# Kernel optimization log

Hardware: AMD Instinct MI355X
Metric: run time of the kernel (lower is better)

Reference implementation:

```python
import jax, jax.numpy as jnp
import numpy as np

N, E, D, H, C, ED = 30000, 300000, 256, 8, 32, 32
HID = H * C  # 256 = hidden_channels


def setup_inputs() -> dict:
    key = jax.random.key(0)
    ks = jax.random.split(key, 14)
    w = lambda k, shp, fan: (jax.random.normal(k, shp, jnp.float32) / np.sqrt(fan)).astype(jnp.float32)
    return {
        "x": jax.random.normal(ks[0], (N, D), jnp.float32),
        "edge_index": jax.random.randint(ks[1], (2, E), 0, N, jnp.int32),
        "edge_attr": jax.random.normal(ks[2], (E, ED), jnp.float32),
        # TransformerConv params (PyG: q/k/v Linears have bias; lin_edge & lin_skip bias=False)
        "Wq": w(ks[3], (D, HID), D), "bq": 0.01 * jax.random.normal(ks[4], (HID,), jnp.float32),
        "Wk": w(ks[5], (D, HID), D), "bk": 0.01 * jax.random.normal(ks[6], (HID,), jnp.float32),
        "Wv": w(ks[7], (D, HID), D), "bv": 0.01 * jax.random.normal(ks[8], (HID,), jnp.float32),
        "We": w(ks[9], (ED, HID), ED),
        "Wskip": w(ks[10], (D, HID), D),
        # MLP([HID, HID, HID], gelu-tanh, plain_last=False): two Linear+act layers
        "W1": w(ks[11], (HID, HID), HID), "b1": jnp.zeros((HID,), jnp.float32),
        "W2": w(ks[12], (HID, HID), HID), "b2": jnp.zeros((HID,), jnp.float32),
    }


def reference(x, edge_index, edge_attr, Wq, bq, Wk, bk, Wv, bv, We, Wskip, W1, b1, W2, b2):
    src, dst = edge_index[0], edge_index[1]  # message flows src -> dst
    q = (x @ Wq + bq).reshape(N, H, C)
    k = (x @ Wk + bk).reshape(N, H, C)
    v = (x @ Wv + bv).reshape(N, H, C)
    e = (edge_attr @ We).reshape(E, H, C)
    k_e = k[src] + e                               # [E,H,C]
    v_e = v[src] + e                               # [E,H,C]
    logits = jnp.einsum('ehc,ehc->eh', q[dst], k_e) / np.sqrt(C)  # [E,H]
    # segment softmax over incoming edges of each dst node
    m = jax.ops.segment_max(logits, dst, num_segments=N)          # [N,H]
    a = jnp.exp(logits - m[dst])
    denom = jax.ops.segment_sum(a, dst, num_segments=N)           # [N,H]
    alpha = a / (denom[dst] + 1e-16)                              # [E,H]
    agg = jax.ops.segment_sum(alpha[:, :, None] * v_e, dst, num_segments=N)  # [N,H,C]
    out = agg.reshape(N, HID) + x @ Wskip          # concat heads + root skip
    # residual MLP: x + gelu(gelu(x W1 + b1) W2 + b2)
    h = jax.nn.gelu(out @ W1 + b1, approximate=True)
    h = jax.nn.gelu(h @ W2 + b2, approximate=True)
    return out + h
```

## Files before the change

kernel.cpp:

```cpp
#include <hip/hip_runtime.h>

#define NN 30000
#define NE 300000
#define HIDDEN 256

typedef __attribute__((ext_vector_type(8))) __bf16 bf16x8;
typedef __attribute__((ext_vector_type(4))) __bf16 bf16x4;
typedef __attribute__((ext_vector_type(4))) float float4v;

__device__ inline __bf16 f2bf(float f) {
  unsigned u = __builtin_bit_cast(unsigned, f);
  u += 0x7fffu + ((u >> 16) & 1u);
  unsigned short s = (unsigned short)(u >> 16);
  return __builtin_bit_cast(__bf16, s);
}
__device__ inline float bf2f(__bf16 b) {
  unsigned short s = __builtin_bit_cast(unsigned short, b);
  unsigned u = ((unsigned)s) << 16;
  return __builtin_bit_cast(float, u);
}
__device__ inline float gelu_tanh(float x) {
  float x3 = x * x * x;
  return 0.5f * x * (1.0f + tanhf(0.79788456080286536f * (x + 0.044715f * x3)));
}

#define PREP_XB_END (1829 + (NN * 32 + 255) / 256)
__global__ __launch_bounds__(256) void prep_kernel(
    const float* __restrict__ Wq, const float* __restrict__ Wk, const float* __restrict__ Wv,
    const float* __restrict__ Wsk, const float* __restrict__ W1, const float* __restrict__ W2,
    const float* __restrict__ We, const float* __restrict__ bq, const float* __restrict__ bk,
    const float* __restrict__ bv, const float* __restrict__ x,
    __bf16* __restrict__ WTall, __bf16* __restrict__ WT1, __bf16* __restrict__ WT2,
    float* __restrict__ ball, float* __restrict__ WeT, __bf16* __restrict__ xb,
    int* __restrict__ degz) {
  const int b = blockIdx.x;
  const int tid = threadIdx.x;
  if (b < 1792) {
    const int region = b >> 8;
    const int idx = ((b & 255) << 8) | tid;
    const int k = idx & 255, n = idx >> 8;
    float v;
    if (region == 3) {
      const int h = n >> 5, d = n & 31;
      const float* wq = Wq + (size_t)k * 256 + h * 32;
      const float* we = We + (size_t)d * 256 + h * 32;
      float s = 0.f;
#pragma unroll
      for (int c = 0; c < 32; ++c) s += wq[c] * we[c];
      v = s;
    } else {
      const float* W = (region == 0) ? Wq : (region == 1) ? Wk : (region == 2) ? Wv
                     : (region == 4) ? Wsk : (region == 5) ? W1 : W2;
      v = W[(size_t)k * 256 + n];
    }
    const __bf16 bv16 = f2bf(v);
    if (region < 5) WTall[(size_t)region * 65536 + idx] = bv16;
    else if (region == 5) WT1[idx] = bv16;
    else WT2[idx] = bv16;
  } else if (b < 1797) {
    const int j = (b - 1792) * 256 + tid;
    if (j < 1280) {
      float v = 0.f;
      if (j < 256) v = bq[j];
      else if (j < 512) v = bk[j - 256];
      else if (j < 768) v = bv[j - 512];
      else if (j < 1024) {
        const int col = j - 768, h = col >> 5, d = col & 31;
        const float* bqh = bq + h * 32;
        const float* we = We + (size_t)d * 256 + h * 32;
        float s = 0.f;
#pragma unroll
        for (int c = 0; c < 32; ++c) s += bqh[c] * we[c];
        v = s;
      }
      ball[j] = v;
    }
  } else if (b < 1829) {
    const int idx = (b - 1797) * 256 + tid;
    const int ch = idx >> 5, d = idx & 31;
    WeT[idx] = We[(size_t)d * 256 + ch];
  } else if (b < PREP_XB_END) {
    const int t = (b - 1829) * 256 + tid;
    if (t < NN * 256 / 8) {
      const float* p = x + (size_t)t * 8;
      float4v f0 = *(const float4v*)(p);
      float4v f1 = *(const float4v*)(p + 4);
      bf16x8 o;
#pragma unroll
      for (int j = 0; j < 4; ++j) { o[j] = f2bf(f0[j]); o[j + 4] = f2bf(f1[j]); }
      *(bf16x8*)(xb + (size_t)t * 8) = o;
    }
  } else {
    const int idx = (b - PREP_XB_END) * 256 + tid;
    if (idx < 2 * NN) degz[idx] = 0;
  }
}

__global__ void count_deg_kernel(const int* __restrict__ dst, int* __restrict__ deg, int E) {
  int e = blockIdx.x * 256 + threadIdx.x;
  if (e < E) atomicAdd(&deg[dst[e]], 1);
}

__global__ __launch_bounds__(256) void offs_fused_kernel(const int* __restrict__ deg,
                                                         int* __restrict__ offs, int n) {
  __shared__ int tmp[256];
  __shared__ int sbase[4];
  const int t = threadIdx.x;
  const int lim = blockIdx.x * 256;
  int bp = 0;
  for (int idx = t; idx < lim; idx += 256) bp += deg[idx];
#pragma unroll
  for (int s = 1; s < 64; s <<= 1) bp += __shfl_xor(bp, s);
  if ((t & 63) == 0) sbase[t >> 6] = bp;
  const int i = lim + t;
  int v = (i < n) ? deg[i] : 0;
  tmp[t] = v;
  __syncthreads();
  const int base = sbase[0] + sbase[1] + sbase[2] + sbase[3];
  for (int s = 1; s < 256; s <<= 1) {
    int u = (t >= s) ? tmp[t - s] : 0;
    __syncthreads();
    tmp[t] += u;
    __syncthreads();
  }
  if (i < n) offs[i] = base + tmp[t] - v;
  if (blockIdx.x == gridDim.x - 1 && t == 0) offs[n] = NE;
}

__global__ void scatter_kernel(const int* __restrict__ srcIn, const int* __restrict__ dstIn,
                               const float* __restrict__ ea,
                               const int* __restrict__ offs, int* __restrict__ cursor,
                               int* __restrict__ srcs, __bf16* __restrict__ eaC, int E) {
  int e = blockIdx.x * 256 + threadIdx.x;
  if (e >= E) return;
  const float* src = ea + (size_t)e * 32;
  float4v f[8];
#pragma unroll
  for (int t = 0; t < 8; ++t) f[t] = *(const float4v*)(src + t * 4);
  int d = dstIn[e];
  int p = atomicAdd(&cursor[d], 1);
  int o = offs[d] + p;
  srcs[o] = srcIn[e];
  __bf16* dstp = eaC + (size_t)o * 32;
#pragma unroll
  for (int t = 0; t < 4; ++t) {
    bf16x8 b;
#pragma unroll
    for (int j = 0; j < 4; ++j) { b[j] = f2bf(f[t * 2][j]); b[j + 4] = f2bf(f[t * 2 + 1][j]); }
    *(bf16x8*)(dstp + t * 8) = b;
  }
}

template <int GX, int EPI, int MODE>
__global__ __launch_bounds__(256) void gemm_k4(
    const __bf16* __restrict__ A, const __bf16* __restrict__ Wt,
    const float* __restrict__ bias,
    float* __restrict__ Yf, __bf16* __restrict__ Ybf,
    __bf16* __restrict__ QGp, __bf16* __restrict__ KVp,
    const float* __restrict__ resid, int M, int gyTiles) {
  __shared__ char smem[128 * 264 * 2];
  __bf16* Bs = (__bf16*)smem;
  const int bid = blockIdx.x;
  const int stripe = bid / (8 * GX);
  const int rem = bid % (8 * GX);
  const int y8 = rem % 8;
  const int xt = rem / 8;
  const int y = stripe * 8 + y8;
  if (y >= gyTiles) return;
  const int n0 = xt * 128;

  {
    const int t = threadIdx.x;
#pragma unroll
    for (int i = 0; i < 16; ++i) {
      int g = i * 256 + t;
      int row = g >> 5;
      int c16 = g & 31;
      bf16x8 v = *(const bf16x8*)(Wt + (size_t)(n0 + row) * 256 + c16 * 8);
      *(bf16x8*)(Bs + row * 264 + c16 * 8) = v;
    }
  }
  __syncthreads();

  const int lane = threadIdx.x & 63;
  const int w = threadIdx.x >> 6;
  const int r = lane & 15;
  const int q = lane >> 4;
  const int mw = y * 128 + w * 32;
  int ar0 = mw + r;      if (ar0 >= M) ar0 = M - 1;
  int ar1 = mw + 16 + r; if (ar1 >= M) ar1 = M - 1;
  const int kq = q * 8;

  float4v acc[2][8];
#pragma unroll
  for (int i = 0; i < 2; ++i)
#pragma unroll
    for (int t = 0; t < 8; ++t) acc[i][t] = (float4v){0.f, 0.f, 0.f, 0.f};

#pragma unroll
  for (int kk = 0; kk < 256; kk += 32) {
    const int ka = kk + kq;
    bf16x8 a0 = *(const bf16x8*)(A + (size_t)ar0 * 256 + ka);
    bf16x8 a1 = *(const bf16x8*)(A + (size_t)ar1 * 256 + ka);
    bf16x8 b[8];
#pragma unroll
    for (int t = 0; t < 8; ++t)
      b[t] = *(const bf16x8*)(Bs + (t * 16 + r) * 264 + ka);
#pragma unroll
    for (int t = 0; t < 8; ++t) {
      acc[0][t] = __builtin_amdgcn_mfma_f32_16x16x32_bf16(a0, b[t], acc[0][t], 0, 0, 0);
      acc[1][t] = __builtin_amdgcn_mfma_f32_16x16x32_bf16(a1, b[t], acc[1][t], 0, 0, 0);
    }
  }
  __syncthreads();

  float* cs = (float*)smem + w * 4224;
#pragma unroll
  for (int t = 0; t < 8; ++t) {
    const int col = n0 + t * 16 + r;
    const float bb = bias ? bias[col] : 0.0f;
#pragma unroll
    for (int i2 = 0; i2 < 2; ++i2)
#pragma unroll
      for (int ii = 0; ii < 4; ++ii) {
        float v = acc[i2][t][ii] + bb;
        if constexpr (EPI == 2 || EPI == 3) v = gelu_tanh(v);
        cs[(i2 * 16 + q * 4 + ii) * 132 + t * 16 + r] = v;
      }
  }

  constexpr int NSTR = GX * 128;
  const int p = n0 >> 8;
  const int cbase = n0 & 255;
  __bf16* dstI = (p == 0 || p == 3) ? QGp : KVp;
  const int moff = (p >= 2) ? 4 : 0;
#pragma unroll
  for (int i = 0; i < 16; ++i) {
    const int rl = i * 2 + (lane >> 5);
    const int row = mw + rl;
    const int c4 = (lane & 31) * 4;
    float4v v = *(const float4v*)(cs + rl * 132 + c4);
    if (row < M) {
      if constexpr (MODE == 1) {
        if (p == 4) {
          *(float4v*)(Yf + (size_t)row * 256 + cbase + c4) = v;
        } else {
          bf16x4 b4;
          b4[0] = f2bf(v[0]); b4[1] = f2bf(v[1]); b4[2] = f2bf(v[2]); b4[3] = f2bf(v[3]);
          const int c = cbase + c4;
          *(bf16x4*)(dstI + (size_t)row * 512 + 2 * c + moff) = b4;
        }
      } else if constexpr (EPI == 1) {
        *(float4v*)(Yf + (size_t)row * NSTR + n0 + c4) = v;
      } else if constexpr (EPI == 3) {
        float4v rr = *(const float4v*)(resid + (size_t)row * NSTR + n0 + c4);
        v[0] += rr[0]; v[1] += rr[1]; v[2] += rr[2]; v[3] += rr[3];
        *(float4v*)(Yf + (size_t)row * NSTR + n0 + c4) = v;
      } else {
        bf16x4 b4;
        b4[0] = f2bf(v[0]); b4[1] = f2bf(v[1]); b4[2] = f2bf(v[2]); b4[3] = f2bf(v[3]);
        *(bf16x4*)(Ybf + (size_t)row * NSTR + n0 + c4) = b4;
      }
    }
  }
}

__global__ __launch_bounds__(256) void attn_kernel(
    const __bf16* __restrict__ QG, const __bf16* __restrict__ KV,
    const __bf16* __restrict__ eaC,
    const int* __restrict__ srcs, const int* __restrict__ offs,
    float* __restrict__ OUT, __bf16* __restrict__ AE) {
  __shared__ float sdn[4][64];
  __shared__ float sav[4][64][4], sae[4][64][4];
  const int lane = threadIdx.x & 63;
  const int w = threadIdx.x >> 6;
  const int n = blockIdx.x;
  const int sub = lane & 7;
  const int ch = w * 64 + lane;

  const int beg = offs[n], end = offs[n + 1];
  const float opre = OUT[(size_t)n * 256 + ch];

  const float LSC = 0.25506589858f;
  const bf16x8 qg = *(const bf16x8*)(QG + (size_t)n * 512 + lane * 8);
  const float q0 = bf2f(qg[0]) * LSC, q1 = bf2f(qg[1]) * LSC;
  const float q2 = bf2f(qg[2]) * LSC, q3 = bf2f(qg[3]) * LSC;
  const float g0 = bf2f(qg[4]) * LSC, g1 = bf2f(qg[5]) * LSC;
  const float g2 = bf2f(qg[6]) * LSC, g3 = bf2f(qg[7]) * LSC;

  float denom = 0.f;
  float4v accv = {0.f, 0.f, 0.f, 0.f};
  float4v acce = {0.f, 0.f, 0.f, 0.f};

  for (int b0 = beg; b0 < end; b0 += 64) {
    const int rem = end - b0;
    const int cnt = (rem < 64) ? rem : 64;
    const int sl = (lane < cnt) ? lane : cnt - 1;
    const int myS = srcs[b0 + sl];

    int j = w;
    for (; j + 4 < cnt; j += 8) {
      const int s0 = __builtin_amdgcn_readlane(myS, j);
      const int s1 = __builtin_amdgcn_readlane(myS, j + 4);
      const bf16x8 kv0 = *(const bf16x8*)(KV + (size_t)s0 * 512 + lane * 8);
      const bf16x4 a0 = *(const bf16x4*)(eaC + (size_t)(b0 + j) * 32 + sub * 4);
      const bf16x8 kv1 = *(const bf16x8*)(KV + (size_t)s1 * 512 + lane * 8);
      const bf16x4 a1 = *(const bf16x4*)(eaC + (size_t)(b0 + j + 4) * 32 + sub * 4);
      const float e00 = bf2f(a0[0]), e01 = bf2f(a0[1]), e02 = bf2f(a0[2]), e03 = bf2f(a0[3]);
      const float e10 = bf2f(a1[0]), e11 = bf2f(a1[1]), e12 = bf2f(a1[2]), e13 = bf2f(a1[3]);
      float p0 = q0 * bf2f(kv0[0]) + q1 * bf2f(kv0[1]) + q2 * bf2f(kv0[2]) + q3 * bf2f(kv0[3])
               + g0 * e00 + g1 * e01 + g2 * e02 + g3 * e03;
      float p1 = q0 * bf2f(kv1[0]) + q1 * bf2f(kv1[1]) + q2 * bf2f(kv1[2]) + q3 * bf2f(kv1[3])
               + g0 * e10 + g1 * e11 + g2 * e12 + g3 * e13;
      p0 += __shfl_xor(p0, 1); p1 += __shfl_xor(p1, 1);
      p0 += __shfl_xor(p0, 2); p1 += __shfl_xor(p1, 2);
      p0 += __shfl_xor(p0, 4); p1 += __shfl_xor(p1, 4);
      const float w0 = exp2f(p0);
      const float w1 = exp2f(p1);
      denom += w0 + w1;
      accv[0] += w0 * bf2f(kv0[4]) + w1 * bf2f(kv1[4]);
      accv[1] += w0 * bf2f(kv0[5]) + w1 * bf2f(kv1[5]);
      accv[2] += w0 * bf2f(kv0[6]) + w1 * bf2f(kv1[6]);
      accv[3] += w0 * bf2f(kv0[7]) + w1 * bf2f(kv1[7]);
      acce[0] += w0 * e00 + w1 * e10;
      acce[1] += w0 * e01 + w1 * e11;
      acce[2] += w0 * e02 + w1 * e12;
      acce[3] += w0 * e03 + w1 * e13;
    }
    if (j < cnt) {
      const int s0 = __builtin_amdgcn_readlane(myS, j);
      const bf16x8 kv0 = *(const bf16x8*)(KV + (size_t)s0 * 512 + lane * 8);
      const bf16x4 a0 = *(const bf16x4*)(eaC + (size_t)(b0 + j) * 32 + sub * 4);
      const float e00 = bf2f(a0[0]), e01 = bf2f(a0[1]), e02 = bf2f(a0[2]), e03 = bf2f(a0[3]);
      float p0 = q0 * bf2f(kv0[0]) + q1 * bf2f(kv0[1]) + q2 * bf2f(kv0[2]) + q3 * bf2f(kv0[3])
               + g0 * e00 + g1 * e01 + g2 * e02 + g3 * e03;
      p0 += __shfl_xor(p0, 1);
      p0 += __shfl_xor(p0, 2);
      p0 += __shfl_xor(p0, 4);
      const float w0 = exp2f(p0);
      denom += w0;
      accv[0] += w0 * bf2f(kv0[4]);
      accv[1] += w0 * bf2f(kv0[5]);
      accv[2] += w0 * bf2f(kv0[6]);
      accv[3] += w0 * bf2f(kv0[7]);
      acce[0] += w0 * e00;
      acce[1] += w0 * e01;
      acce[2] += w0 * e02;
      acce[3] += w0 * e03;
    }
  }

  sdn[w][lane] = denom;
#pragma unroll
  for (int j = 0; j < 4; ++j) { sav[w][lane][j] = accv[j]; sae[w][lane][j] = acce[j]; }
  __syncthreads();

  const int lp = ch >> 2, jp = ch & 3;
  const float D = sdn[0][lp] + sdn[1][lp] + sdn[2][lp] + sdn[3][lp];
  const float av = sav[0][lp][jp] + sav[1][lp][jp] + sav[2][lp][jp] + sav[3][lp][jp];
  const float ae = sae[0][lp][jp] + sae[1][lp][jp] + sae[2][lp][jp] + sae[3][lp][jp];
  const float inv = 1.0f / (D + 1e-16f);
  OUT[(size_t)n * 256 + ch] = opre + av * inv;
  AE[(size_t)n * 256 + ch] = f2bf(ae * inv);
}

__global__ __launch_bounds__(256) void post_kernel(
    const __bf16* __restrict__ AE, const float* __restrict__ WeT,
    float* __restrict__ OUT, __bf16* __restrict__ OUTh) {
  const int lane = threadIdx.x & 63;
  const int wave = threadIdx.x >> 6;
  const int c0 = lane * 4;
  const int hg = lane >> 3;

  float4v w4[4][8];
#pragma unroll
  for (int j = 0; j < 4; ++j)
#pragma unroll
    for (int s = 0; s < 8; ++s)
      w4[j][s] = *(const float4v*)(WeT + (size_t)(c0 + j) * 32 + s * 4);

  const int nbase = blockIdx.x * 64;
  for (int it = 0; it < 16; ++it) {
    const int n = nbase + it * 4 + wave;
    if (n >= NN) return;
    const __bf16* aerow = AE + (size_t)n * HIDDEN + hg * 32;
    float aef[32];
#pragma unroll
    for (int t = 0; t < 4; ++t) {
      bf16x8 a8 = *(const bf16x8*)(aerow + t * 8);
#pragma unroll
      for (int j = 0; j < 8; ++j) aef[t * 8 + j] = bf2f(a8[j]);
    }
    float4v o = *(const float4v*)(OUT + (size_t)n * HIDDEN + c0);
#pragma unroll
    for (int j = 0; j < 4; ++j) {
      float s = 0.f;
#pragma unroll
      for (int g = 0; g < 8; ++g) {
        s += aef[g * 4 + 0] * w4[j][g][0] + aef[g * 4 + 1] * w4[j][g][1]
           + aef[g * 4 + 2] * w4[j][g][2] + aef[g * 4 + 3] * w4[j][g][3];
      }
      o[j] += s;
    }
    *(float4v*)(OUT + (size_t)n * HIDDEN + c0) = o;
    bf16x4 ob;
    ob[0] = f2bf(o[0]); ob[1] = f2bf(o[1]); ob[2] = f2bf(o[2]); ob[3] = f2bf(o[3]);
    *(bf16x4*)(OUTh + (size_t)n * HIDDEN + c0) = ob;
  }
}

extern "C" void kernel_launch(void* const* d_in, const int* in_sizes, int n_in,
                              void* d_out, int out_size, void* d_ws, size_t ws_size,
                              hipStream_t stream) {
  (void)in_sizes; (void)n_in; (void)out_size; (void)ws_size;
  const float* x   = (const float*)d_in[0];
  const int*   ei  = (const int*)d_in[1];
  const float* ea  = (const float*)d_in[2];
  const float* Wq  = (const float*)d_in[3];
  const float* bq  = (const float*)d_in[4];
  const float* Wk  = (const float*)d_in[5];
  const float* bk  = (const float*)d_in[6];
  const float* Wv  = (const float*)d_in[7];
  const float* bv  = (const float*)d_in[8];
  const float* We  = (const float*)d_in[9];
  const float* Wsk = (const float*)d_in[10];
  const float* W1  = (const float*)d_in[11];
  const float* b1  = (const float*)d_in[12];
  const float* W2  = (const float*)d_in[13];
  const float* b2  = (const float*)d_in[14];
  float* out = (float*)d_out;

  char* ws = (char*)d_ws;
  size_t off = 0;
  auto alloc = [&](size_t bytes) -> char* {
    off = (off + 255) & ~(size_t)255;
    char* p = ws + off;
    off += bytes;
    return p;
  };
  __bf16* QG   = (__bf16*)alloc((size_t)NN * 512 * 2);
  __bf16* KV   = (__bf16*)alloc((size_t)NN * 512 * 2);
  __bf16* xb   = (__bf16*)alloc((size_t)NN * 256 * 2);
  __bf16* AE   = (__bf16*)alloc((size_t)NN * 256 * 2);
  __bf16* OUTh = (__bf16*)alloc((size_t)NN * 256 * 2);
  __bf16* eaC  = (__bf16*)alloc((size_t)NE * 32 * 2);
  __bf16* WTall = (__bf16*)alloc((size_t)1280 * 256 * 2);
  __bf16* WT1  = (__bf16*)alloc(256 * 256 * 2);
  __bf16* WT2  = (__bf16*)alloc(256 * 256 * 2);
  float*  ball = (float*)alloc(1280 * 4);
  float*  WeT  = (float*)alloc(256 * 32 * 4);
  int* deg    = (int*)alloc((size_t)2 * NN * 4);
  int* cursor = deg + NN;
  int* offs   = (int*)alloc((size_t)(NN + 1) * 4);
  int* srcs   = (int*)alloc((size_t)NE * 4);
  __bf16* H1 = AE;

  const int* srcIn = ei;
  const int* dstIn = ei + NE;

  const int prepBlocks = PREP_XB_END + (2 * NN + 255) / 256;
  prep_kernel<<<prepBlocks, 256, 0, stream>>>(Wq, Wk, Wv, Wsk, W1, W2, We, bq, bk, bv, x,
                                              WTall, WT1, WT2, ball, WeT, xb, deg);

  const int nb = (NN + 255) / 256;
  count_deg_kernel<<<(NE + 255) / 256, 256, 0, stream>>>(dstIn, deg, NE);
  offs_fused_kernel<<<nb, 256, 0, stream>>>(deg, offs, NN);
  scatter_kernel<<<(NE + 255) / 256, 256, 0, stream>>>(srcIn, dstIn, ea, offs, cursor,
                                                       srcs, eaC, NE);

  const int gy = (NN + 127) / 128;
  const int stripes = (gy + 7) / 8;
  gemm_k4<10, 0, 1><<<stripes * 80, 256, 0, stream>>>(
      xb, WTall, ball, out, nullptr, QG, KV, nullptr, NN, gy);

  attn_kernel<<<NN, 256, 0, stream>>>(QG, KV, eaC, srcs, offs, out, AE);

  post_kernel<<<(NN + 63) / 64, 256, 0, stream>>>(AE, WeT, out, OUTh);

  gemm_k4<2, 2, 0><<<stripes * 16, 256, 0, stream>>>(
      OUTh, WT1, b1, nullptr, H1, nullptr, nullptr, nullptr, NN, gy);
  gemm_k4<2, 3, 0><<<stripes * 16, 256, 0, stream>>>(
      H1, WT2, b2, out, nullptr, nullptr, nullptr, out, NN, gy);
}
```

Measured before the change: 368.6 us.

## Fuse edge-attr projection epilogue into attention kernel and drop readlane batching

The post_kernel, which projects the aggregated edge-attribute sum through We and adds it to the output, is folded into the attention kernel's epilogue. Wave 0 reduces the partial sums, broadcasts per-head values with shuffles, multiplies by WeT rows loaded from global memory, and writes OUT plus its bf16 copy directly. This removes the AE intermediate round-trip and one kernel launch. The edge loop also reads srcs per edge instead of loading 64 indices per batch and using readlane. The cost is a serialized epilogue on one wave per block and repeated WeT loads per node, which may hurt occupancy or latency.

```diff
diff --git a/kernel.cpp b/kernel.cpp
--- a/kernel.cpp
+++ b/kernel.cpp
@@ -269,17 +269,14 @@
     const __bf16* __restrict__ QG, const __bf16* __restrict__ KV,
     const __bf16* __restrict__ eaC,
     const int* __restrict__ srcs, const int* __restrict__ offs,
-    float* __restrict__ OUT, __bf16* __restrict__ AE) {
+    const float* __restrict__ WeT,
+    float* __restrict__ OUT, __bf16* __restrict__ OUTh) {
   __shared__ float sdn[4][64];
   __shared__ float sav[4][64][4], sae[4][64][4];
   const int lane = threadIdx.x & 63;
   const int w = threadIdx.x >> 6;
   const int n = blockIdx.x;
   const int sub = lane & 7;
-  const int ch = w * 64 + lane;
-
-  const int beg = offs[n], end = offs[n + 1];
-  const float opre = OUT[(size_t)n * 256 + ch];
 
   const float LSC = 0.25506589858f;
   const bf16x8 qg = *(const bf16x8*)(QG + (size_t)n * 512 + lane * 8);
@@ -291,121 +288,104 @@
   float denom = 0.f;
   float4v accv = {0.f, 0.f, 0.f, 0.f};
   float4v acce = {0.f, 0.f, 0.f, 0.f};
-
-  for (int b0 = beg; b0 < end; b0 += 64) {
-    const int rem = end - b0;
-    const int cnt = (rem < 64) ? rem : 64;
-    const int sl = (lane < cnt) ? lane : cnt - 1;
-    const int myS = srcs[b0 + sl];
-
-    int j = w;
-    for (; j + 4 < cnt; j += 8) {
-      const int s0 = __builtin_amdgcn_readlane(myS, j);
-      const int s1 = __builtin_amdgcn_readlane(myS, j + 4);
-      const bf16x8 kv0 = *(const bf16x8*)(KV + (size_t)s0 * 512 + lane * 8);
-      const bf16x4 a0 = *(const bf16x4*)(eaC + (size_t)(b0 + j) * 32 + sub * 4);
-      const bf16x8 kv1 = *(const bf16x8*)(KV + (size_t)s1 * 512 + lane * 8);
-      const bf16x4 a1 = *(const bf16x4*)(eaC + (size_t)(b0 + j + 4) * 32 + sub * 4);
-      const float e00 = bf2f(a0[0]), e01 = bf2f(a0[1]), e02 = bf2f(a0[2]), e03 = bf2f(a0[3]);
-      const float e10 = bf2f(a1[0]), e11 = bf2f(a1[1]), e12 = bf2f(a1[2]), e13 = bf2f(a1[3]);
-      float p0 = q0 * bf2f(kv0[0]) + q1 * bf2f(kv0[1]) + q2 * bf2f(kv0[2]) + q3 * bf2f(kv0[3])
-               + g0 * e00 + g1 * e01 + g2 * e02 + g3 * e03;
-      float p1 = q0 * bf2f(kv1[0]) + q1 * bf2f(kv1[1]) + q2 * bf2f(kv1[2]) + q3 * bf2f(kv1[3])
-               + g0 * e10 + g1 * e11 + g2 * e12 + g3 * e13;
-      p0 += __shfl_xor(p0, 1); p1 += __shfl_xor(p1, 1);
-      p0 += __shfl_xor(p0, 2); p1 += __shfl_xor(p1, 2);
-      p0 += __shfl_xor(p0, 4); p1 += __shfl_xor(p1, 4);
-      const float w0 = exp2f(p0);
-      const float w1 = exp2f(p1);
-      denom += w0 + w1;
-      accv[0] += w0 * bf2f(kv0[4]) + w1 * bf2f(kv1[4]);
-      accv[1] += w0 * bf2f(kv0[5]) + w1 * bf2f(kv1[5]);
-      accv[2] += w0 * bf2f(kv0[6]) + w1 * bf2f(kv1[6]);
-      accv[3] += w0 * bf2f(kv0[7]) + w1 * bf2f(kv1[7]);
-      acce[0] += w0 * e00 + w1 * e10;
-      acce[1] += w0 * e01 + w1 * e11;
-      acce[2] += w0 * e02 + w1 * e12;
-      acce[3] += w0 * e03 + w1 * e13;
-    }
-    if (j < cnt) {
-      const int s0 = __builtin_amdgcn_readlane(myS, j);
-      const bf16x8 kv0 = *(const bf16x8*)(KV + (size_t)s0 * 512 + lane * 8);
-      const bf16x4 a0 = *(const bf16x4*)(eaC + (size_t)(b0 + j) * 32 + sub * 4);
-      const float e00 = bf2f(a0[0]), e01 = bf2f(a0[1]), e02 = bf2f(a0[2]), e03 = bf2f(a0[3]);
-      float p0 = q0 * bf2f(kv0[0]) + q1 * bf2f(kv0[1]) + q2 * bf2f(kv0[2]) + q3 * bf2f(kv0[3])
-               + g0 * e00 + g1 * e01 + g2 * e02 + g3 * e03;
-      p0 += __shfl_xor(p0, 1);
-      p0 += __shfl_xor(p0, 2);
-      p0 += __shfl_xor(p0, 4);
-      const float w0 = exp2f(p0);
-      denom += w0;
-      accv[0] += w0 * bf2f(kv0[4]);
-      accv[1] += w0 * bf2f(kv0[5]);
-      accv[2] += w0 * bf2f(kv0[6]);
-      accv[3] += w0 * bf2f(kv0[7]);
-      acce[0] += w0 * e00;
-      acce[1] += w0 * e01;
-      acce[2] += w0 * e02;
-      acce[3] += w0 * e03;
-    }
+  const int beg = offs[n], end = offs[n + 1];
+
+  int i = beg + w;
+  for (; i + 4 < end; i += 8) {
+    const int s0 = srcs[i];
+    const int s1 = srcs[i + 4];
+    const bf16x8 kv0 = *(const bf16x8*)(KV + (size_t)s0 * 512 + lane * 8);
+    const bf16x4 a0 = *(const bf16x4*)(eaC + (size_t)i * 32 + sub * 4);
+    const bf16x8 kv1 = *(const bf16x8*)(KV + (size_t)s1 * 512 + lane * 8);
+    const bf16x4 a1 = *(const bf16x4*)(eaC + (size_t)(i + 4) * 32 + sub * 4);
+    const float e00 = bf2f(a0[0]), e01 = bf2f(a0[1]), e02 = bf2f(a0[2]), e03 = bf2f(a0[3]);
+    const float e10 = bf2f(a1[0]), e11 = bf2f(a1[1]), e12 = bf2f(a1[2]), e13 = bf2f(a1[3]);
+    float p0 = q0 * bf2f(kv0[0]) + q1 * bf2f(kv0[1]) + q2 * bf2f(kv0[2]) + q3 * bf2f(kv0[3])
+             + g0 * e00 + g1 * e01 + g2 * e02 + g3 * e03;
+    float p1 = q0 * bf2f(kv1[0]) + q1 * bf2f(kv1[1]) + q2 * bf2f(kv1[2]) + q3 * bf2f(kv1[3])
+             + g0 * e10 + g1 * e11 + g2 * e12 + g3 * e13;
+    p0 += __shfl_xor(p0, 1); p1 += __shfl_xor(p1, 1);
+    p0 += __shfl_xor(p0, 2); p1 += __shfl_xor(p1, 2);
+    p0 += __shfl_xor(p0, 4); p1 += __shfl_xor(p1, 4);
+    const float w0 = exp2f(p0);
+    const float w1 = exp2f(p1);
+    denom += w0 + w1;
+    accv[0] += w0 * bf2f(kv0[4]) + w1 * bf2f(kv1[4]);
+    accv[1] += w0 * bf2f(kv0[5]) + w1 * bf2f(kv1[5]);
+    accv[2] += w0 * bf2f(kv0[6]) + w1 * bf2f(kv1[6]);
+    accv[3] += w0 * bf2f(kv0[7]) + w1 * bf2f(kv1[7]);
+    acce[0] += w0 * e00 + w1 * e10;
+    acce[1] += w0 * e01 + w1 * e11;
+    acce[2] += w0 * e02 + w1 * e12;
+    acce[3] += w0 * e03 + w1 * e13;
+  }
+  if (i < end) {
+    const int s0 = srcs[i];
+    const bf16x8 kv0 = *(const bf16x8*)(KV + (size_t)s0 * 512 + lane * 8);
+    const bf16x4 a0 = *(const bf16x4*)(eaC + (size_t)i * 32 + sub * 4);
+    const float e00 = bf2f(a0[0]), e01 = bf2f(a0[1]), e02 = bf2f(a0[2]), e03 = bf2f(a0[3]);
+    float p0 = q0 * bf2f(kv0[0]) + q1 * bf2f(kv0[1]) + q2 * bf2f(kv0[2]) + q3 * bf2f(kv0[3])
+             + g0 * e00 + g1 * e01 + g2 * e02 + g3 * e03;
+    p0 += __shfl_xor(p0, 1);
+    p0 += __shfl_xor(p0, 2);
+    p0 += __shfl_xor(p0, 4);
+    const float w0 = exp2f(p0);
+    denom += w0;
+    accv[0] += w0 * bf2f(kv0[4]);
+    accv[1] += w0 * bf2f(kv0[5]);
+    accv[2] += w0 * bf2f(kv0[6]);
+    accv[3] += w0 * bf2f(kv0[7]);
+    acce[0] += w0 * e00;
+    acce[1] += w0 * e01;
+    acce[2] += w0 * e02;
+    acce[3] += w0 * e03;
   }
 
   sdn[w][lane] = denom;
 #pragma unroll
   for (int j = 0; j < 4; ++j) { sav[w][lane][j] = accv[j]; sae[w][lane][j] = acce[j]; }
   __syncthreads();
-
-  const int lp = ch >> 2, jp = ch & 3;
-  const float D = sdn[0][lp] + sdn[1][lp] + sdn[2][lp] + sdn[3][lp];
-  const float av = sav[0][lp][jp] + sav[1][lp][jp] + sav[2][lp][jp] + sav[3][lp][jp];
-  const float ae = sae[0][lp][jp] + sae[1][lp][jp] + sae[2][lp][jp] + sae[3][lp][jp];
-  const float inv = 1.0f / (D + 1e-16f);
-  OUT[(size_t)n * 256 + ch] = opre + av * inv;
-  AE[(size_t)n * 256 + ch] = f2bf(ae * inv);
-}
-
-__global__ __launch_bounds__(256) void post_kernel(
-    const __bf16* __restrict__ AE, const float* __restrict__ WeT,
-    float* __restrict__ OUT, __bf16* __restrict__ OUTh) {
-  const int lane = threadIdx.x & 63;
-  const int wave = threadIdx.x >> 6;
-  const int c0 = lane * 4;
-  const int hg = lane >> 3;
-
-  float4v w4[4][8];
-#pragma unroll
-  for (int j = 0; j < 4; ++j)
-#pragma unroll
-    for (int s = 0; s < 8; ++s)
-      w4[j][s] = *(const float4v*)(WeT + (size_t)(c0 + j) * 32 + s * 4);
-
-  const int nbase = blockIdx.x * 64;
-  for (int it = 0; it < 16; ++it) {
-    const int n = nbase + it * 4 + wave;
-    if (n >= NN) return;
-    const __bf16* aerow = AE + (size_t)n * HIDDEN + hg * 32;
-    float aef[32];
-#pragma unroll
-    for (int t = 0; t < 4; ++t) {
-      bf16x8 a8 = *(const bf16x8*)(aerow + t * 8);
-#pragma unroll
-      for (int j = 0; j < 8; ++j) aef[t * 8 + j] = bf2f(a8[j]);
-    }
-    float4v o = *(const float4v*)(OUT + (size_t)n * HIDDEN + c0);
+  if (w == 0) {
+    float D = 0.f;
+    float4v av = {0.f, 0.f, 0.f, 0.f};
+    float4v ae = {0.f, 0.f, 0.f, 0.f};
+#pragma unroll
+    for (int ww = 0; ww < 4; ++ww) {
+      D += sdn[ww][lane];
+#pragma unroll
+      for (int j = 0; j < 4; ++j) { av[j] += sav[ww][lane][j]; ae[j] += sae[ww][lane][j]; }
+    }
+    const float inv = 1.0f / (D + 1e-16f);
+    float aej[4];
+#pragma unroll
+    for (int j = 0; j < 4; ++j) aej[j] = ae[j] * inv;
+
+    const int gb = (lane >> 3) << 3;
+    float aeh[32];
+#pragma unroll
+    for (int g = 0; g < 8; ++g) {
+#pragma unroll
+      for (int k = 0; k < 4; ++k) aeh[g * 4 + k] = __shfl(aej[k], gb + g);
+    }
+
+    const int c0 = lane * 4;
+    float4v o = *(const float4v*)(OUT + (size_t)n * 256 + c0);
 #pragma unroll
     for (int j = 0; j < 4; ++j) {
       float s = 0.f;
+      const float* wr = WeT + (size_t)(c0 + j) * 32;
 #pragma unroll
       for (int g = 0; g < 8; ++g) {
-        s += aef[g * 4 + 0] * w4[j][g][0] + aef[g * 4 + 1] * w4[j][g][1]
-           + aef[g * 4 + 2] * w4[j][g][2] + aef[g * 4 + 3] * w4[j][g][3];
+        float4v w4 = *(const float4v*)(wr + g * 4);
+        s += aeh[g * 4 + 0] * w4[0] + aeh[g * 4 + 1] * w4[1]
+           + aeh[g * 4 + 2] * w4[2] + aeh[g * 4 + 3] * w4[3];
       }
-      o[j] += s;
-    }
-    *(float4v*)(OUT + (size_t)n * HIDDEN + c0) = o;
+      o[j] += av[j] * inv + s;
+    }
+    *(float4v*)(OUT + (size_t)n * 256 + c0) = o;
     bf16x4 ob;
     ob[0] = f2bf(o[0]); ob[1] = f2bf(o[1]); ob[2] = f2bf(o[2]); ob[3] = f2bf(o[3]);
-    *(bf16x4*)(OUTh + (size_t)n * HIDDEN + c0) = ob;
+    *(bf16x4*)(OUTh + (size_t)n * 256 + c0) = ob;
   }
 }
 
@@ -441,7 +421,7 @@
   __bf16* QG   = (__bf16*)alloc((size_t)NN * 512 * 2);
   __bf16* KV   = (__bf16*)alloc((size_t)NN * 512 * 2);
   __bf16* xb   = (__bf16*)alloc((size_t)NN * 256 * 2);
-  __bf16* AE   = (__bf16*)alloc((size_t)NN * 256 * 2);
+  __bf16* H1   = (__bf16*)alloc((size_t)NN * 256 * 2);
   __bf16* OUTh = (__bf16*)alloc((size_t)NN * 256 * 2);
   __bf16* eaC  = (__bf16*)alloc((size_t)NE * 32 * 2);
   __bf16* WTall = (__bf16*)alloc((size_t)1280 * 256 * 2);
@@ -453,7 +433,6 @@
   int* cursor = deg + NN;
   int* offs   = (int*)alloc((size_t)(NN + 1) * 4);
   int* srcs   = (int*)alloc((size_t)NE * 4);
-  __bf16* H1 = AE;
 
   const int* srcIn = ei;
   const int* dstIn = ei + NE;
@@ -473,9 +452,7 @@
   gemm_k4<10, 0, 1><<<stripes * 80, 256, 0, stream>>>(
       xb, WTall, ball, out, nullptr, QG, KV, nullptr, NN, gy);
 
-  attn_kernel<<<NN, 256, 0, stream>>>(QG, KV, eaC, srcs, offs, out, AE);
-
-  post_kernel<<<(NN + 63) / 64, 256, 0, stream>>>(AE, WeT, out, OUTh);
+  attn_kernel<<<NN, 256, 0, stream>>>(QG, KV, eaC, srcs, offs, WeT, out, OUTh);
 
   gemm_k4<2, 2, 0><<<stripes * 16, 256, 0, stream>>>(
       OUTh, WT1, b1, nullptr, H1, nullptr, nullptr, nullptr, NN, gy);
```

Result: slower. 457.9 us (+24.3%).
